# Kernel tuning notes

Hardware: AMD Instinct MI355X
Metric: run time of the kernel (lower is better)

Reference implementation:

```python
import jax, jax.numpy as jnp
import numpy as np

B, S, D = 4, 4096, 1024
EPS_LN = 1e-5
EPS_REC = 1e-8


def _layernorm(x, g, b):
    mu = jnp.mean(x, axis=-1, keepdims=True)
    var = jnp.mean((x - mu) ** 2, axis=-1, keepdims=True)
    return (x - mu) * jax.lax.rsqrt(var + EPS_LN) * g + b


def setup_inputs() -> dict:
    key = jax.random.key(0)
    ks = jax.random.split(key, 8)
    scale = 1.0 / np.sqrt(D)
    return {
        "x": jax.random.normal(ks[0], (B, S, D), dtype=jnp.float32),
        "x_prev": jax.random.normal(ks[1], (B, S, D), dtype=jnp.float32),
        "mu": jnp.float32(0.5),
        "decay_w": jax.random.uniform(ks[2], (D, 1), jnp.float32, -scale, scale),
        "decay_b": jnp.zeros((1,), jnp.float32),
        "ln1_g": jnp.ones((D,), jnp.float32),
        "ln1_b": jnp.zeros((D,), jnp.float32),
        "Wr_w": jax.random.uniform(ks[3], (D, D), jnp.float32, -scale, scale),
        "Wr_b": jnp.zeros((D,), jnp.float32),
        "Wv_w": jax.random.uniform(ks[4], (D, D), jnp.float32, -scale, scale),
        "Wv_b": jnp.zeros((D,), jnp.float32),
        "ln2_g": jnp.ones((D,), jnp.float32),
        "ln2_b": jnp.zeros((D,), jnp.float32),
    }


def reference(x, x_prev, mu, decay_w, decay_b, ln1_g, ln1_b,
              Wr_w, Wr_b, Wv_w, Wv_b, ln2_g, ln2_b):
    # Shift (token-mix by scalar mu)
    shifted = mu * x + (1.0 - mu) * x_prev  # [B,S,D]

    # SequenceMergingSeq with C = V = W = shifted
    decay = jax.nn.sigmoid(jnp.einsum("bsd,do->bso", shifted, decay_w) + decay_b)  # [B,S,1]
    e = jnp.exp(shifted)                       # [B,S,D]
    ea = jnp.sum(e, axis=-1, keepdims=True)    # [B,S,1]
    ev = e * shifted                           # [B,S,D]

    def step(carry, inp):
        a, b = carry
        d_t, ea_t, ev_t = inp
        a = d_t * a + ea_t            # [B,1]
        b = d_t * b + ev_t            # [B,D]
        return (a, b), b / (a + EPS_REC)

    init = (jnp.zeros((B, 1), shifted.dtype), jnp.zeros((B, D), shifted.dtype))
    xs = (jnp.swapaxes(decay, 0, 1), jnp.swapaxes(ea, 0, 1), jnp.swapaxes(ev, 0, 1))
    _, out_sbd = jax.lax.scan(step, init, xs)  # [S,B,D]
    merged = _layernorm(jnp.swapaxes(out_sbd, 0, 1), ln1_g, ln1_b)  # [B,S,D]

    # StateCoupling
    gate = jax.nn.sigmoid(jnp.einsum("bsd,ed->bse", merged, Wr_w) + Wr_b)
    value = jnp.einsum("bsd,ed->bse", merged, Wv_w) + Wv_b
    coupled = _layernorm(gate * value, ln2_g, ln2_b)

    return shifted + coupled
```

## Files before the change

### kernel.cpp

```cpp
#include <hip/hip_runtime.h>

#define BATCH 4
#define SEQ   4096
#define DIM   1024
#define NCH   512
#define CHK   8
#define NROWS (BATCH*SEQ)
#define NTG   16

typedef __attribute__((ext_vector_type(4))) float f32x4;
typedef __attribute__((ext_vector_type(8))) short shortx8;
typedef __attribute__((ext_vector_type(4))) short shortx4;

static __device__ __forceinline__ unsigned short f2bf(float f){
    unsigned int u = __float_as_uint(f);
    u += 0x7FFFu + ((u >> 16) & 1u);
    return (unsigned short)(u >> 16);
}
static __device__ __forceinline__ float bf2f(unsigned short h){
    return __uint_as_float(((unsigned int)h) << 16);
}
static __device__ __forceinline__ float sigmoidf_fast(float x){
    return 1.0f / (1.0f + __expf(-x));
}
static __device__ __forceinline__ shortx4 pack4(f32x4 s){
    shortx4 o;
    o.x = (short)f2bf(s.x); o.y = (short)f2bf(s.y);
    o.z = (short)f2bf(s.z); o.w = (short)f2bf(s.w);
    return o;
}
static __device__ __forceinline__ f32x4 unpack4(shortx4 s){
    f32x4 o;
    o.x = bf2f((unsigned short)s.x); o.y = bf2f((unsigned short)s.y);
    o.z = bf2f((unsigned short)s.z); o.w = bf2f((unsigned short)s.w);
    return o;
}

__global__ __launch_bounds__(256) void k_shift_scan(
    const float* __restrict__ X, const float* __restrict__ XP,
    const float* __restrict__ mu_p, const float* __restrict__ dw,
    const float* __restrict__ db_p,
    const float* __restrict__ Wr, const float* __restrict__ Wv,
    unsigned short* __restrict__ Wcat,
    unsigned short* __restrict__ shifted,
    unsigned short* __restrict__ b_local, float* __restrict__ a_local,
    float* __restrict__ cumP)
{
    const int tid  = threadIdx.x;

    if (blockIdx.x >= 512){
        const int pb = blockIdx.x - 512;
        #pragma unroll 4
        for (int i = 0; i < 32; ++i){
            const int n = pb*32 + i;
            const int grp = n >> 5, r = n & 31;
            const float* src = (r < 16) ? (Wr + (size_t)(grp*16 + r)*DIM)
                                        : (Wv + (size_t)(grp*16 + (r-16))*DIM);
            f32x4 v = reinterpret_cast<const f32x4*>(src)[tid];
            reinterpret_cast<shortx4*>(Wcat)[n*256 + tid] = pack4(v);
        }
        return;
    }

    const int lane = tid & 63;
    const int wid  = tid >> 6;
    const int cid  = blockIdx.x*4 + wid;
    const int batch = cid >> 9;
    const int chunk = cid & (NCH-1);
    const int row0  = batch*SEQ + chunk*CHK;

    const float mu = mu_p[0];
    const float om = 1.0f - mu;
    const float db = db_p[0];

    const f32x4* dwv = reinterpret_cast<const f32x4*>(dw);
    const f32x4 w0 = dwv[lane], w1 = dwv[64+lane], w2 = dwv[128+lane], w3 = dwv[192+lane];

    f32x4 b0 = {0,0,0,0}, b1 = {0,0,0,0}, b2 = {0,0,0,0}, b3 = {0,0,0,0};
    float a_run = 0.f, cp = 1.f;

    const f32x4* Xv  = reinterpret_cast<const f32x4*>(X);
    const f32x4* XPv = reinterpret_cast<const f32x4*>(XP);
    shortx4* BL = reinterpret_cast<shortx4*>(b_local);
    shortx4* SH = reinterpret_cast<shortx4*>(shifted);

    for (int r = 0; r < CHK; ++r){
        const int row = row0 + r;
        const int rb  = row*(DIM/4);

        f32x4 x0 = Xv[rb+lane],     x1 = Xv[rb+64+lane],
              x2 = Xv[rb+128+lane], x3 = Xv[rb+192+lane];
        f32x4 p0 = XPv[rb+lane],     p1 = XPv[rb+64+lane],
              p2 = XPv[rb+128+lane], p3 = XPv[rb+192+lane];
        f32x4 s0 = mu*x0 + om*p0, s1 = mu*x1 + om*p1;
        f32x4 s2 = mu*x2 + om*p2, s3 = mu*x3 + om*p3;

        SH[rb+lane]     = pack4(s0);
        SH[rb+64+lane]  = pack4(s1);
        SH[rb+128+lane] = pack4(s2);
        SH[rb+192+lane] = pack4(s3);

        float dot = s0.x*w0.x + s0.y*w0.y + s0.z*w0.z + s0.w*w0.w
                  + s1.x*w1.x + s1.y*w1.y + s1.z*w1.z + s1.w*w1.w
                  + s2.x*w2.x + s2.y*w2.y + s2.z*w2.z + s2.w*w2.w
                  + s3.x*w3.x + s3.y*w3.y + s3.z*w3.z + s3.w*w3.w;

        f32x4 e0, e1, e2, e3;
        e0.x=__expf(s0.x); e0.y=__expf(s0.y); e0.z=__expf(s0.z); e0.w=__expf(s0.w);
        e1.x=__expf(s1.x); e1.y=__expf(s1.y); e1.z=__expf(s1.z); e1.w=__expf(s1.w);
        e2.x=__expf(s2.x); e2.y=__expf(s2.y); e2.z=__expf(s2.z); e2.w=__expf(s2.w);
        e3.x=__expf(s3.x); e3.y=__expf(s3.y); e3.z=__expf(s3.z); e3.w=__expf(s3.w);
        float ea = e0.x+e0.y+e0.z+e0.w + e1.x+e1.y+e1.z+e1.w
                 + e2.x+e2.y+e2.z+e2.w + e3.x+e3.y+e3.z+e3.w;

        #pragma unroll
        for (int off = 1; off < 64; off <<= 1){
            dot += __shfl_xor(dot, off, 64);
            ea  += __shfl_xor(ea,  off, 64);
        }

        const float dt = sigmoidf_fast(dot + db);
        a_run = dt*a_run + ea;
        cp   *= dt;
        b0 = dt*b0 + e0*s0;  b1 = dt*b1 + e1*s1;
        b2 = dt*b2 + e2*s2;  b3 = dt*b3 + e3*s3;

        BL[rb+lane]     = pack4(b0);
        BL[rb+64+lane]  = pack4(b1);
        BL[rb+128+lane] = pack4(b2);
        BL[rb+192+lane] = pack4(b3);
        if (lane == 0){ a_local[row] = a_run; cumP[row] = cp; }
    }
}

__global__ __launch_bounds__(64) void k_combine(
    const unsigned short* __restrict__ b_local, const float* __restrict__ a_local,
    const float* __restrict__ cumP,
    float* __restrict__ carryA, unsigned short* __restrict__ carryB)
{
    const int batch = blockIdx.x >> 2;
    const int dseg  = blockIdx.x & 3;
    const int tid = threadIdx.x;
    const int d0 = dseg*256 + tid*4;

    __shared__ float sP[NCH], sA[NCH];
    for (int c = tid; c < NCH; c += 64){
        const int er = batch*SEQ + c*CHK + (CHK-1);
        sP[c] = cumP[er];
        sA[c] = a_local[er];
    }
    __syncthreads();

    const unsigned short* bl = b_local + (size_t)batch*SEQ*DIM + d0;
    unsigned short* cB = carryB + (size_t)batch*NCH*DIM + d0;
    const bool wA = (dseg == 0 && tid == 0);
    float* cAp = carryA + batch*NCH;

    shortx4 pf[16];
    #pragma unroll
    for (int i = 0; i < 16; ++i)
        pf[i] = *reinterpret_cast<const shortx4*>(bl + (i*CHK + CHK-1)*DIM);

    f32x4 cb = {0,0,0,0};
    float ca = 0.f;

    for (int cc = 0; cc < NCH; cc += 16){
        const bool more = (cc + 16 < NCH);
        #pragma unroll
        for (int k = 0; k < 16; ++k){
            const int c = cc + k;
            f32x4 v = unpack4(pf[k]);
            if (more)
                pf[k] = *reinterpret_cast<const shortx4*>(bl + ((c+16)*CHK + CHK-1)*DIM);
            *reinterpret_cast<shortx4*>(cB + (size_t)c*DIM) = pack4(cb);
            if (wA) cAp[c] = ca;
            const float p = sP[c];
            cb = p*cb + v;
            ca = p*ca + sA[c];
        }
    }
}

__global__ __launch_bounds__(256) void k_fix_ln1(
    const unsigned short* __restrict__ b_local, const float* __restrict__ a_local,
    const float* __restrict__ cumP, const float* __restrict__ carryA,
    const unsigned short* __restrict__ carryB,
    const float* __restrict__ g1, const float* __restrict__ bb1,
    unsigned short* __restrict__ merged)
{
    const int tid = threadIdx.x, lane = tid & 63, wid = tid >> 6;
    const int row = blockIdx.x*4 + wid;
    const int batch = row >> 12;
    const int c = (row & (SEQ-1)) >> 3;

    const float cpv = cumP[row];
    const float a = a_local[row] + cpv * carryA[batch*NCH + c];
    const float inv_a = 1.0f / (a + 1e-8f);

    const shortx4* BL = reinterpret_cast<const shortx4*>(b_local) + (size_t)row*256;
    const shortx4* CB = reinterpret_cast<const shortx4*>(carryB) + (size_t)(batch*NCH + c)*256;

    f32x4 o[4];
    float s = 0.f, s2 = 0.f;
    #pragma unroll
    for (int j = 0; j < 4; ++j){
        f32x4 bl = unpack4(BL[j*64 + lane]);
        f32x4 cb = unpack4(CB[j*64 + lane]);
        f32x4 v = (bl + cpv*cb) * inv_a;
        o[j] = v;
        s  += v.x+v.y+v.z+v.w;
        s2 += v.x*v.x + v.y*v.y + v.z*v.z + v.w*v.w;
    }
    #pragma unroll
    for (int off = 1; off < 64; off <<= 1){
        s  += __shfl_xor(s,  off, 64);
        s2 += __shfl_xor(s2, off, 64);
    }
    const float mean = s * (1.0f/DIM);
    const float rstd = rsqrtf(s2*(1.0f/DIM) - mean*mean + 1e-5f);
    shortx4* MG = reinterpret_cast<shortx4*>(merged) + (size_t)row*256;
    #pragma unroll
    for (int j = 0; j < 4; ++j){
        f32x4 gg = reinterpret_cast<const f32x4*>(g1)[j*64 + lane];
        f32x4 bb = reinterpret_cast<const f32x4*>(bb1)[j*64 + lane];
        MG[j*64 + lane] = pack4((o[j] - mean)*rstd*gg + bb);
    }
}

typedef __attribute__((address_space(3))) unsigned int lds_uint;
typedef __attribute__((address_space(1))) unsigned int glob_uint;
static __device__ __forceinline__ void gload16(const unsigned short* g, char* l){
    __builtin_amdgcn_global_load_lds((const glob_uint*)g, (lds_uint*)l, 16, 0, 0);
}
#define SBAR() do { __builtin_amdgcn_sched_barrier(0); __builtin_amdgcn_s_barrier(); __builtin_amdgcn_sched_barrier(0); } while(0)
#define LGKM0() do { asm volatile("s_waitcnt lgkmcnt(0)" ::: "memory"); __builtin_amdgcn_sched_barrier(0); } while(0)
#define VMC(n)  asm volatile("s_waitcnt vmcnt(" #n ")" ::: "memory")
#define LDSE 136

__global__ __launch_bounds__(512, 2) void k_gemm(
    const unsigned short* __restrict__ A,
    const unsigned short* __restrict__ Bt,
    const float* __restrict__ rbias, const float* __restrict__ vbias,
    unsigned short* __restrict__ gv)
{
    __shared__ __align__(16) char lds[131072];
    const int tid  = threadIdx.x;
    const int lane = tid & 63;
    const int wid  = tid >> 6;
    const int wqm  = wid >> 2;
    const int wqn  = wid & 3;

    const int bid  = blockIdx.x;
    const int wgid = (bid & 7)*64 + (bid >> 3);
    const int mt = wgid >> 3, nt = wgid & 7;
    const int m0 = mt*256, n0 = nt*256;

    const int rin = lane >> 2;
    const int scg = (lane & 3) ^ (((lane >> 5) & 1) << 1);
    const unsigned short* gA = A  + (size_t)(m0 + wid*16 + rin)*DIM + scg*8;
    const unsigned short* gB = Bt + (size_t)(n0 + wid*16 + rin)*DIM + scg*8;

    const int fr = lane & 15, fq = lane >> 4;
    const int soff = fr*64 + ((fq*16) ^ ((fr & 8) ? 32 : 0));

    f32x4 acc0[8], acc1[8], acc2[8], acc3[8];
    #pragma unroll
    for (int i = 0; i < 8; ++i){
        acc0[i] = (f32x4){0,0,0,0}; acc1[i] = (f32x4){0,0,0,0};
        acc2[i] = (f32x4){0,0,0,0}; acc3[i] = (f32x4){0,0,0,0};
    }

    auto STAGE = [&](int Tk, int piece){
        const int isA = (piece == 0 || piece == 3);
        const int h   = (piece >= 2) ? 1 : 0;
        char* dst = lds + (Tk & 1)*65536 + (isA ? 0 : 32768) + h*16384 + wid*2048;
        const unsigned short* s = (isA ? gA : gB) + (size_t)(h*128)*DIM + Tk*64;
        gload16(s,      dst);
        gload16(s + 32, dst + 1024);
    };

    shortx8 aA[8], bB0[4], bB1[4];
    auto LOAD_A = [&](const char* base){
        #pragma unroll
        for (int rf = 0; rf < 4; ++rf)
            #pragma unroll
            for (int kb = 0; kb < 2; ++kb)
                aA[rf*2+kb] = *reinterpret_cast<const shortx8*>(
                    base + (wqm*4 + rf)*2048 + kb*1024 + soff);
    };
    auto LOAD_B = [&](const char* base, shortx8* dst){
        #pragma unroll
        for (int cf = 0; cf < 2; ++cf)
            #pragma unroll
            for (int kb = 0; kb < 2; ++kb)
                dst[cf*2+kb] = *reinterpret_cast<const shortx8*>(
                    base + (wqn*2 + cf)*2048 + kb*1024 + soff);
    };

    #define MFMA16(ACC, BX)                                                     \
        __builtin_amdgcn_s_setprio(1);                                          \
        _Pragma("unroll")                                                       \
        for (int rf = 0; rf < 4; ++rf)                                          \
            _Pragma("unroll")                                                   \
            for (int cf = 0; cf < 2; ++cf){                                     \
                ACC[rf*2+cf] = __builtin_amdgcn_mfma_f32_16x16x32_bf16(         \
                    aA[rf*2+0], BX[cf*2+0], ACC[rf*2+cf], 0,0,0);               \
                ACC[rf*2+cf] = __builtin_amdgcn_mfma_f32_16x16x32_bf16(         \
                    aA[rf*2+1], BX[cf*2+1], ACC[rf*2+cf], 0,0,0);               \
            }                                                                   \
        __builtin_amdgcn_s_setprio(0);

    STAGE(0,0); STAGE(0,1); STAGE(0,2); STAGE(0,3);
    VMC(4);
    SBAR();

    for (int T = 0; T < NTG; ++T){
        const char* cb = lds + (T & 1)*65536;
        const bool hn = (T + 1 < NTG);

        LOAD_A(cb);
        LOAD_B(cb + 32768, bB0);
        if (hn) STAGE(T+1, 0);
        if (hn) { VMC(4); } else { VMC(2); }
        SBAR();
        LGKM0();
        MFMA16(acc0, bB0);
        SBAR();

        LOAD_B(cb + 49152, bB1);
        if (hn) STAGE(T+1, 1);
        if (hn) { VMC(4); } else { VMC(0); }
        SBAR();
        LGKM0();
        MFMA16(acc1, bB1);
        SBAR();

        LOAD_A(cb + 16384);
        if (hn) STAGE(T+1, 2);
        if (hn) { VMC(4); }
        SBAR();
        LGKM0();
        MFMA16(acc3, bB1);
        SBAR();

        if (hn) STAGE(T+1, 3);
        if (hn) { VMC(4); }
        SBAR();
        MFMA16(acc2, bB0);
        SBAR();
    }

    __syncthreads();
    unsigned short* ep = reinterpret_cast<unsigned short*>(lds);
    #pragma unroll
    for (int q = 0; q < 4; ++q){
        const f32x4* ac = (q==0) ? acc0 : (q==1) ? acc1 : (q==2) ? acc2 : acc3;
        const int QM = q >> 1, QN = q & 1;
        const int el = QN*64 + wqn*16 + fr;
        const float rbe = rbias[nt*128 + el];
        const float vbe = vbias[nt*128 + el];
        #pragma unroll
        for (int rf = 0; rf < 4; ++rf){
            const int rbase = QM*128 + wqm*64 + rf*16 + fq*4;
            f32x4 ga = ac[rf*2+0], va = ac[rf*2+1];
            #pragma unroll
            for (int qq = 0; qq < 4; ++qq){
                const float g = sigmoidf_fast(ga[qq] + rbe);
                ep[(rbase + qq)*LDSE + el] = f2bf(g*(va[qq] + vbe));
            }
        }
    }
    __syncthreads();
    #pragma unroll
    for (int p = 0; p < 8; ++p){
        const int r  = p*32 + (tid >> 4);
        const int c8 = tid & 15;
        shortx8 val = *reinterpret_cast<const shortx8*>(&ep[r*LDSE + c8*8]);
        *reinterpret_cast<shortx8*>(&gv[(size_t)(m0 + r)*DIM + nt*128 + c8*8]) = val;
    }
    #undef MFMA16
}

__global__ __launch_bounds__(256) void k_ln2_res(
    const unsigned short* __restrict__ gvb, const unsigned short* __restrict__ shifted,
    const float* __restrict__ g2, const float* __restrict__ b2,
    float* __restrict__ out)
{
    const int tid = threadIdx.x, lane = tid & 63, wid = tid >> 6;
    const int row = blockIdx.x*4 + wid;

    const shortx4* GV = reinterpret_cast<const shortx4*>(gvb) + (size_t)row*256;
    const shortx4* SH = reinterpret_cast<const shortx4*>(shifted) + (size_t)row*256;

    f32x4 v[4];
    float s = 0.f, s2 = 0.f;
    #pragma unroll
    for (int j = 0; j < 4; ++j){
        f32x4 x = unpack4(GV[j*64 + lane]);
        v[j] = x;
        s  += x.x+x.y+x.z+x.w;
        s2 += x.x*x.x + x.y*x.y + x.z*x.z + x.w*x.w;
    }
    #pragma unroll
    for (int off = 1; off < 64; off <<= 1){
        s  += __shfl_xor(s,  off, 64);
        s2 += __shfl_xor(s2, off, 64);
    }
    const float mean = s * (1.0f/DIM);
    const float rstd = rsqrtf(s2*(1.0f/DIM) - mean*mean + 1e-5f);
    f32x4* O = reinterpret_cast<f32x4*>(out) + (size_t)row*256;
    #pragma unroll
    for (int j = 0; j < 4; ++j){
        f32x4 gg = reinterpret_cast<const f32x4*>(g2)[j*64 + lane];
        f32x4 bb = reinterpret_cast<const f32x4*>(b2)[j*64 + lane];
        f32x4 sh = unpack4(SH[j*64 + lane]);
        O[j*64 + lane] = sh + (v[j] - mean)*rstd*gg + bb;
    }
}

extern "C" void kernel_launch(void* const* d_in, const int* in_sizes, int n_in,
                              void* d_out, int out_size, void* d_ws, size_t ws_size,
                              hipStream_t stream)
{
    (void)in_sizes; (void)n_in; (void)out_size; (void)ws_size;
    const float* x     = (const float*)d_in[0];
    const float* xprev = (const float*)d_in[1];
    const float* mu    = (const float*)d_in[2];
    const float* dw    = (const float*)d_in[3];
    const float* db    = (const float*)d_in[4];
    const float* ln1g  = (const float*)d_in[5];
    const float* ln1b  = (const float*)d_in[6];
    const float* Wr    = (const float*)d_in[7];
    const float* Wrb   = (const float*)d_in[8];
    const float* Wv    = (const float*)d_in[9];
    const float* Wvb   = (const float*)d_in[10];
    const float* ln2g  = (const float*)d_in[11];
    const float* ln2b  = (const float*)d_in[12];
    float* out = (float*)d_out;

    char* ws = (char*)d_ws;
    size_t off = 0;
    auto alloc = [&](size_t bytes) -> void* {
        void* p = ws + off;
        off += (bytes + 255) & ~(size_t)255;
        return p;
    };
    unsigned short* shifted = (unsigned short*)alloc((size_t)NROWS*DIM*2);
    unsigned short* b_local = (unsigned short*)alloc((size_t)NROWS*DIM*2);
    unsigned short* merged  = (unsigned short*)alloc((size_t)NROWS*DIM*2);
    unsigned short* carryB  = (unsigned short*)alloc((size_t)BATCH*NCH*DIM*2);
    unsigned short* Wcat    = (unsigned short*)alloc((size_t)2048*1024*2);
    float* a_local          = (float*)alloc((size_t)NROWS*4);
    float* cumP             = (float*)alloc((size_t)NROWS*4);
    float* carryA           = (float*)alloc((size_t)BATCH*NCH*4);
    unsigned short* gvbuf   = b_local;

    hipLaunchKernelGGL(k_shift_scan, dim3(576),  dim3(256), 0, stream,
                       x, xprev, mu, dw, db, Wr, Wv, Wcat, shifted, b_local, a_local, cumP);
    hipLaunchKernelGGL(k_combine,    dim3(16),   dim3(64),  0, stream,
                       b_local, a_local, cumP, carryA, carryB);
    hipLaunchKernelGGL(k_fix_ln1,    dim3(4096), dim3(256), 0, stream,
                       b_local, a_local, cumP, carryA, carryB, ln1g, ln1b, merged);
    hipLaunchKernelGGL(k_gemm,       dim3(512),  dim3(512), 0, stream,
                       merged, Wcat, Wrb, Wvb, gvbuf);
    hipLaunchKernelGGL(k_ln2_res,    dim3(4096), dim3(256), 0, stream,
                       gvbuf, shifted, ln2g, ln2b, out);
}
```

Before: 206.0 us.

## Restructure GEMM main loop to K=32 steps with register double-buffered fragments

The fused gate/value GEMM kernel now walks K in 32 steps of 32 instead of 16 steps of 64, with a two-deep LDS ring of 32KB each instead of 64KB buffers. Each wave holds a full 128x64 accumulator tile and ping-pongs two register fragment sets, so the LDS reads for the next step are issued before the current step's MFMAs. Prefetch runs two K-steps ahead and there are fewer barriers per MFMA block. The intent is better overlap of LDS reads and global loads with MFMA work and a smaller LDS footprint, in exchange for more registers from the doubled fragment sets.

```diff
diff --git a/kernel.cpp b/kernel.cpp
--- a/kernel.cpp
+++ b/kernel.cpp
@@ -6,7 +6,7 @@
 #define NCH   512
 #define CHK   8
 #define NROWS (BATCH*SEQ)
-#define NTG   16
+#define NKT   32
 
 typedef __attribute__((ext_vector_type(4))) float f32x4;
 typedef __attribute__((ext_vector_type(8))) short shortx8;
@@ -243,12 +243,12 @@
     const float* __restrict__ rbias, const float* __restrict__ vbias,
     unsigned short* __restrict__ gv)
 {
-    __shared__ __align__(16) char lds[131072];
+    __shared__ __align__(16) char lds[69632];
     const int tid  = threadIdx.x;
     const int lane = tid & 63;
     const int wid  = tid >> 6;
-    const int wqm  = wid >> 2;
-    const int wqn  = wid & 3;
+    const int wm   = wid >> 2;
+    const int wn   = wid & 3;
 
     const int bid  = blockIdx.x;
     const int wgid = (bid & 7)*64 + (bid >> 3);
@@ -257,116 +257,87 @@
 
     const int rin = lane >> 2;
     const int scg = (lane & 3) ^ (((lane >> 5) & 1) << 1);
-    const unsigned short* gA = A  + (size_t)(m0 + wid*16 + rin)*DIM + scg*8;
-    const unsigned short* gB = Bt + (size_t)(n0 + wid*16 + rin)*DIM + scg*8;
+    const unsigned short* gA = A  + (size_t)(m0 + wid*32 + rin)*DIM + scg*8;
+    const unsigned short* gB = Bt + (size_t)(n0 + wid*32 + rin)*DIM + scg*8;
 
     const int fr = lane & 15, fq = lane >> 4;
     const int soff = fr*64 + ((fq*16) ^ ((fr & 8) ? 32 : 0));
 
-    f32x4 acc0[8], acc1[8], acc2[8], acc3[8];
-    #pragma unroll
-    for (int i = 0; i < 8; ++i){
-        acc0[i] = (f32x4){0,0,0,0}; acc1[i] = (f32x4){0,0,0,0};
-        acc2[i] = (f32x4){0,0,0,0}; acc3[i] = (f32x4){0,0,0,0};
-    }
-
-    auto STAGE = [&](int Tk, int piece){
-        const int isA = (piece == 0 || piece == 3);
-        const int h   = (piece >= 2) ? 1 : 0;
-        char* dst = lds + (Tk & 1)*65536 + (isA ? 0 : 32768) + h*16384 + wid*2048;
-        const unsigned short* s = (isA ? gA : gB) + (size_t)(h*128)*DIM + Tk*64;
-        gload16(s,      dst);
-        gload16(s + 32, dst + 1024);
+    f32x4 acc[8][4];
+    #pragma unroll
+    for (int i = 0; i < 8; ++i)
+        #pragma unroll
+        for (int j = 0; j < 4; ++j) acc[i][j] = (f32x4){0,0,0,0};
+
+    auto STAGE = [&](int tk){
+        char* da = lds + (tk & 1)*32768 + wid*2048;
+        const unsigned short* sa = gA + tk*32;
+        gload16(sa,          da);
+        gload16(sa + 16*DIM, da + 1024);
+        char* db = lds + (tk & 1)*32768 + 16384 + wid*2048;
+        const unsigned short* sb = gB + tk*32;
+        gload16(sb,          db);
+        gload16(sb + 16*DIM, db + 1024);
     };
 
-    shortx8 aA[8], bB0[4], bB1[4];
-    auto LOAD_A = [&](const char* base){
-        #pragma unroll
-        for (int rf = 0; rf < 4; ++rf)
-            #pragma unroll
-            for (int kb = 0; kb < 2; ++kb)
-                aA[rf*2+kb] = *reinterpret_cast<const shortx8*>(
-                    base + (wqm*4 + rf)*2048 + kb*1024 + soff);
-    };
-    auto LOAD_B = [&](const char* base, shortx8* dst){
-        #pragma unroll
-        for (int cf = 0; cf < 2; ++cf)
-            #pragma unroll
-            for (int kb = 0; kb < 2; ++kb)
-                dst[cf*2+kb] = *reinterpret_cast<const shortx8*>(
-                    base + (wqn*2 + cf)*2048 + kb*1024 + soff);
-    };
-
-    #define MFMA16(ACC, BX)                                                     \
+    shortx8 afA[8], bfA[4], afB[8], bfB[4];
+
+    #define LOADF(AF, BF, bb) do {                                              \
+        _Pragma("unroll")                                                       \
+        for (int mf = 0; mf < 8; ++mf)                                          \
+            AF[mf] = *reinterpret_cast<const shortx8*>((bb) + (wm*8 + mf)*1024 + soff); \
+        _Pragma("unroll")                                                       \
+        for (int nf = 0; nf < 4; ++nf)                                          \
+            BF[nf] = *reinterpret_cast<const shortx8*>((bb) + 16384 + (wn*4 + nf)*1024 + soff); \
+    } while (0)
+
+    #define MFMA32(AF, BF) do {                                                 \
         __builtin_amdgcn_s_setprio(1);                                          \
         _Pragma("unroll")                                                       \
-        for (int rf = 0; rf < 4; ++rf)                                          \
+        for (int mf = 0; mf < 8; ++mf)                                          \
             _Pragma("unroll")                                                   \
-            for (int cf = 0; cf < 2; ++cf){                                     \
-                ACC[rf*2+cf] = __builtin_amdgcn_mfma_f32_16x16x32_bf16(         \
-                    aA[rf*2+0], BX[cf*2+0], ACC[rf*2+cf], 0,0,0);               \
-                ACC[rf*2+cf] = __builtin_amdgcn_mfma_f32_16x16x32_bf16(         \
-                    aA[rf*2+1], BX[cf*2+1], ACC[rf*2+cf], 0,0,0);               \
-            }                                                                   \
-        __builtin_amdgcn_s_setprio(0);
-
-    STAGE(0,0); STAGE(0,1); STAGE(0,2); STAGE(0,3);
+            for (int nf = 0; nf < 4; ++nf)                                      \
+                acc[mf][nf] = __builtin_amdgcn_mfma_f32_16x16x32_bf16(          \
+                    AF[mf], BF[nf], acc[mf][nf], 0, 0, 0);                      \
+        __builtin_amdgcn_s_setprio(0);                                          \
+    } while (0)
+
+    #define BODY(T, AFc, BFc, AFn, BFn) do {                                    \
+        LGKM0();                                                                \
+        SBAR();                          \
+        if ((T) + 2 < NKT){ STAGE((T) + 2); VMC(4); }                           \
+        else if ((T) + 2 == NKT){ VMC(0); }                                     \
+        SBAR();                          \
+        if ((T) + 1 < NKT){ LOADF(AFn, BFn, lds + (((T) + 1) & 1)*32768); }     \
+        __builtin_amdgcn_sched_barrier(0);                                      \
+        MFMA32(AFc, BFc);                                                       \
+    } while (0)
+
+    STAGE(0); STAGE(1);
     VMC(4);
     SBAR();
-
-    for (int T = 0; T < NTG; ++T){
-        const char* cb = lds + (T & 1)*65536;
-        const bool hn = (T + 1 < NTG);
-
-        LOAD_A(cb);
-        LOAD_B(cb + 32768, bB0);
-        if (hn) STAGE(T+1, 0);
-        if (hn) { VMC(4); } else { VMC(2); }
-        SBAR();
-        LGKM0();
-        MFMA16(acc0, bB0);
-        SBAR();
-
-        LOAD_B(cb + 49152, bB1);
-        if (hn) STAGE(T+1, 1);
-        if (hn) { VMC(4); } else { VMC(0); }
-        SBAR();
-        LGKM0();
-        MFMA16(acc1, bB1);
-        SBAR();
-
-        LOAD_A(cb + 16384);
-        if (hn) STAGE(T+1, 2);
-        if (hn) { VMC(4); }
-        SBAR();
-        LGKM0();
-        MFMA16(acc3, bB1);
-        SBAR();
-
-        if (hn) STAGE(T+1, 3);
-        if (hn) { VMC(4); }
-        SBAR();
-        MFMA16(acc2, bB0);
-        SBAR();
+    LOADF(afA, bfA, lds);
+
+    for (int T = 0; T < NKT; T += 2){
+        BODY(T,     afA, bfA, afB, bfB);
+        BODY(T + 1, afB, bfB, afA, bfA);
     }
 
     __syncthreads();
     unsigned short* ep = reinterpret_cast<unsigned short*>(lds);
     #pragma unroll
-    for (int q = 0; q < 4; ++q){
-        const f32x4* ac = (q==0) ? acc0 : (q==1) ? acc1 : (q==2) ? acc2 : acc3;
-        const int QM = q >> 1, QN = q & 1;
-        const int el = QN*64 + wqn*16 + fr;
+    for (int pr = 0; pr < 2; ++pr){
+        const int el = wn*32 + pr*16 + fr;
         const float rbe = rbias[nt*128 + el];
         const float vbe = vbias[nt*128 + el];
         #pragma unroll
-        for (int rf = 0; rf < 4; ++rf){
-            const int rbase = QM*128 + wqm*64 + rf*16 + fq*4;
-            f32x4 ga = ac[rf*2+0], va = ac[rf*2+1];
+        for (int mf = 0; mf < 8; ++mf){
+            const int rbase = wm*128 + mf*16 + fq*4;
+            f32x4 ga = acc[mf][2*pr], va = acc[mf][2*pr+1];
             #pragma unroll
-            for (int qq = 0; qq < 4; ++qq){
-                const float g = sigmoidf_fast(ga[qq] + rbe);
-                ep[(rbase + qq)*LDSE + el] = f2bf(g*(va[qq] + vbe));
+            for (int q = 0; q < 4; ++q){
+                const float g = sigmoidf_fast(ga[q] + rbe);
+                ep[(rbase + q)*LDSE + el] = f2bf(g*(va[q] + vbe));
             }
         }
     }
@@ -378,7 +349,9 @@
         shortx8 val = *reinterpret_cast<const shortx8*>(&ep[r*LDSE + c8*8]);
         *reinterpret_cast<shortx8*>(&gv[(size_t)(m0 + r)*DIM + nt*128 + c8*8]) = val;
     }
-    #undef MFMA16
+    #undef BODY
+    #undef MFMA32
+    #undef LOADF
 }
 
 __global__ __launch_bounds__(256) void k_ln2_res(
```

Result: slower. 210.6 us (+2.2%).

## Deepen GEMM LDS pipeline to a ten-slot ring with fewer barriers

Applied to the files above, without the earlier changes.

Replaces the double-buffered LDS staging in the fused gate/value GEMM with a ten-slot ring of 16KB pieces, prefetching two K-steps ahead and unrolling by pairs of K tiles. Each phase now has one barrier instead of two, and vmcnt waits happen only twice per K step. The goal is to hide global load latency better and cut synchronisation overhead. The cost is that LDS grows to 160KB, which likely lowers occupancy from the two-block launch bound to one block per CU.

```diff
diff --git a/kernel.cpp b/kernel.cpp
--- a/kernel.cpp
+++ b/kernel.cpp
@@ -7,6 +7,7 @@
 #define CHK   8
 #define NROWS (BATCH*SEQ)
 #define NTG   16
+#define NPAIR 8
 
 typedef __attribute__((ext_vector_type(4))) float f32x4;
 typedef __attribute__((ext_vector_type(8))) short shortx8;
@@ -243,7 +244,7 @@
     const float* __restrict__ rbias, const float* __restrict__ vbias,
     unsigned short* __restrict__ gv)
 {
-    __shared__ __align__(16) char lds[131072];
+    __shared__ __align__(16) char lds[163840];
     const int tid  = threadIdx.x;
     const int lane = tid & 63;
     const int wid  = tid >> 6;
@@ -270,17 +271,20 @@
         acc2[i] = (f32x4){0,0,0,0}; acc3[i] = (f32x4){0,0,0,0};
     }
 
-    auto STAGE = [&](int Tk, int piece){
-        const int isA = (piece == 0 || piece == 3);
-        const int h   = (piece >= 2) ? 1 : 0;
-        char* dst = lds + (Tk & 1)*65536 + (isA ? 0 : 32768) + h*16384 + wid*2048;
-        const unsigned short* s = (isA ? gA : gB) + (size_t)(h*128)*DIM + Tk*64;
+    auto STAGE_P = [&](int k){
+        if (k >= 4*NTG) return;
+        const int T = k >> 2, pc = k & 3, slot = k % 10;
+        const int isA = (pc == 0 || pc == 3);
+        const int h   = (pc >= 2) ? 1 : 0;
+        char* dst = lds + slot*16384 + wid*2048;
+        const unsigned short* s = (isA ? gA : gB) + (size_t)(h*128)*DIM + T*64;
         gload16(s,      dst);
         gload16(s + 32, dst + 1024);
     };
 
     shortx8 aA[8], bB0[4], bB1[4];
-    auto LOAD_A = [&](const char* base){
+    auto LOAD_A = [&](int slot){
+        const char* base = lds + slot*16384;
         #pragma unroll
         for (int rf = 0; rf < 4; ++rf)
             #pragma unroll
@@ -288,7 +292,8 @@
                 aA[rf*2+kb] = *reinterpret_cast<const shortx8*>(
                     base + (wqm*4 + rf)*2048 + kb*1024 + soff);
     };
-    auto LOAD_B = [&](const char* base, shortx8* dst){
+    auto LOAD_B = [&](int slot, shortx8* dst){
+        const char* base = lds + slot*16384;
         #pragma unroll
         for (int cf = 0; cf < 2; ++cf)
             #pragma unroll
@@ -310,42 +315,56 @@
             }                                                                   \
         __builtin_amdgcn_s_setprio(0);
 
-    STAGE(0,0); STAGE(0,1); STAGE(0,2); STAGE(0,3);
-    VMC(4);
+    #pragma unroll
+    for (int k = 0; k < 8; ++k) STAGE_P(k);
+    VMC(6);
     SBAR();
 
-    for (int T = 0; T < NTG; ++T){
-        const char* cb = lds + (T & 1)*65536;
-        const bool hn = (T + 1 < NTG);
-
-        LOAD_A(cb);
-        LOAD_B(cb + 32768, bB0);
-        if (hn) STAGE(T+1, 0);
-        if (hn) { VMC(4); } else { VMC(2); }
-        SBAR();
+    for (int i = 0; i < NPAIR; ++i){
+        const int T0 = 2*i;
+        const int sA0t0 = (4*T0  ) % 10, sB0t0 = (4*T0+1) % 10;
+        const int sB1t0 = (4*T0+2) % 10, sA1t0 = (4*T0+3) % 10;
+        const int sA0t1 = (4*T0+4) % 10, sB0t1 = (4*T0+5) % 10;
+        const int sB1t1 = (4*T0+6) % 10, sA1t1 = (4*T0+7) % 10;
+        const int P = 8*i;
+        const bool last = (i == NPAIR-1);
+
+        LOAD_A(sA0t0); LOAD_B(sB0t0, bB0);
+        STAGE_P(P + 8);
         LGKM0();
         MFMA16(acc0, bB0);
         SBAR();
-
-        LOAD_B(cb + 49152, bB1);
-        if (hn) STAGE(T+1, 1);
-        if (hn) { VMC(4); } else { VMC(0); }
-        SBAR();
+        LOAD_B(sB1t0, bB1);
+        STAGE_P(P + 9);
         LGKM0();
         MFMA16(acc1, bB1);
         SBAR();
-
-        LOAD_A(cb + 16384);
-        if (hn) STAGE(T+1, 2);
-        if (hn) { VMC(4); }
-        SBAR();
+        LOAD_A(sA1t0);
+        STAGE_P(P + 10);
         LGKM0();
         MFMA16(acc3, bB1);
         SBAR();
-
-        if (hn) STAGE(T+1, 3);
-        if (hn) { VMC(4); }
-        SBAR();
+        STAGE_P(P + 11);
+        if (last) { VMC(0); } else { VMC(6); }
+        MFMA16(acc2, bB0);
+        SBAR();
+        LOAD_A(sA0t1); LOAD_B(sB0t1, bB0);
+        STAGE_P(P + 12);
+        LGKM0();
+        MFMA16(acc0, bB0);
+        SBAR();
+        LOAD_B(sB1t1, bB1);
+        STAGE_P(P + 13);
+        LGKM0();
+        MFMA16(acc1, bB1);
+        SBAR();
+        LOAD_A(sA1t1);
+        STAGE_P(P + 14);
+        LGKM0();
+        MFMA16(acc3, bB1);
+        SBAR();
+        STAGE_P(P + 15);
+        if (!last) { VMC(6); }
         MFMA16(acc2, bB0);
         SBAR();
     }
```

After: 208.1 us. No clear change (+1.0%).
